# Kernel tuning notes

Hardware: AMD Instinct MI355X
Metric: run time of the kernel (lower is better)

The kernel has to match this reference:

```python
import jax, jax.numpy as jnp
import numpy as np

N, P, C, IMG = 65536, 2048, 3, 256


def setup_inputs() -> dict:
    key = jax.random.key(0)
    k1, k2, k3, k4 = jax.random.split(key, 4)
    X = jax.random.randint(k1, (N, 2), 0, IMG, dtype=jnp.int32)
    pattern_layer = jax.random.randint(k2, (P, 2), 0, IMG, dtype=jnp.int32)
    W2 = jax.random.normal(k3, (C, P), dtype=jnp.float32)
    # sigma >= 1 per module docstring; adapt_sigma yields per-node values
    sigmaSq = jax.random.uniform(k4, (P,), dtype=jnp.float32) * 4.0 + 1.0
    return {"X": X, "pattern_layer": pattern_layer, "W2": W2, "sigmaSq": sigmaSq}


def reference(X, pattern_layer, W2, sigmaSq):
    # Squared L2 distance from each query pixel to each pattern node, [N, P].
    # Coords are small ints, so the expanded form is exact in fp32.
    Xf = X.astype(jnp.float32)
    Pf = pattern_layer.astype(jnp.float32)
    Dsq = ((Xf * Xf).sum(-1)[:, None]
           + (Pf * Pf).sum(-1)[None, :]
           - 2.0 * Xf @ Pf.T)
    # Gaussian RBF with per-node bandwidth sigmaSq, [N, P]
    rbf = jnp.exp(-Dsq / (2.0 * sigmaSq))
    den = rbf.sum(axis=1)                       # [N]
    num = jnp.einsum('np,cp->nc', rbf, W2)      # [N, C]
    return num / den[:, None]
```

## Files before the change

### kernel.cpp

```cpp
#include <hip/hip_runtime.h>
#include <math.h>

#ifndef __has_builtin
#define __has_builtin(x) 0
#endif

#define GRIDC  32
#define NCELL  1024
#define CSHIFT 3
#define RAD    4

#define OFF_A 2048
#define OFF_B 10240
#define WS_NEED_INTS (10240 + 4096)

__device__ __forceinline__ float fast_exp2(float x) {
#if __has_builtin(__builtin_amdgcn_exp2f)
    return __builtin_amdgcn_exp2f(x);
#else
    return exp2f(x);
#endif
}

__device__ __forceinline__ int cell_of(int x, int y) {
    int cx = x >> CSHIFT; cx = cx < 0 ? 0 : (cx > GRIDC - 1 ? GRIDC - 1 : cx);
    int cy = y >> CSHIFT; cy = cy < 0 ? 0 : (cy > GRIDC - 1 ? GRIDC - 1 : cy);
    return (cy << 5) + cx;
}

__global__ __launch_bounds__(1024) void bin_nodes(const int* __restrict__ pat,
        const float* __restrict__ W2, const float* __restrict__ sig,
        int* __restrict__ wsI, int P) {
    __shared__ int cnt[NCELL];
    __shared__ int buf[NCELL];
    const int tid = threadIdx.x;
    cnt[tid] = 0;
    __syncthreads();

    int cell0 = -1, slot0 = 0, cell1 = -1, slot1 = 0;
    if (tid < P) {
        cell0 = cell_of(pat[2 * tid], pat[2 * tid + 1]);
        slot0 = atomicAdd(&cnt[cell0], 1);
    }
    const int p1 = tid + 1024;
    if (p1 < P) {
        cell1 = cell_of(pat[2 * p1], pat[2 * p1 + 1]);
        slot1 = atomicAdd(&cnt[cell1], 1);
    }
    __syncthreads();

    const int c = cnt[tid];
    buf[tid] = c;
    __syncthreads();
    for (int off = 1; off < NCELL; off <<= 1) {
        int t = (tid >= off) ? buf[tid - off] : 0;
        __syncthreads();
        buf[tid] += t;
        __syncthreads();
    }
    const int excl = buf[tid] - c;
    wsI[tid] = excl;
    if (tid == NCELL - 1) wsI[NCELL] = buf[tid];
    cnt[tid] = excl;
    __syncthreads();

    float4* __restrict__ A = (float4*)(wsI + OFF_A);
    float2* __restrict__ B = (float2*)(wsI + OFF_B);
    if (cell0 >= 0) {
        int pos = cnt[cell0] + slot0;
        A[pos] = make_float4((float)pat[2 * tid], (float)pat[2 * tid + 1],
                             -0.7213475204444817f / sig[tid], W2[tid]);
        B[pos] = make_float2(W2[P + tid], W2[2 * P + tid]);
    }
    if (cell1 >= 0) {
        int pos = cnt[cell1] + slot1;
        A[pos] = make_float4((float)pat[2 * p1], (float)pat[2 * p1 + 1],
                             -0.7213475204444817f / sig[p1], W2[p1]);
        B[pos] = make_float2(W2[P + p1], W2[2 * P + p1]);
    }
}

__global__ __launch_bounds__(256) void rbf_win(const int* __restrict__ X,
        const int* __restrict__ wsI, float* __restrict__ out, int N, int P) {
    __shared__ float4 sA[2048];
    __shared__ float2 sB[2048];
    __shared__ int    sst[NCELL + 1];
    __shared__ float4 accb[128];

    const int tid = threadIdx.x;
    const float4* __restrict__ A = (const float4*)(wsI + OFF_A);
    const float2* __restrict__ B = (const float2*)(wsI + OFF_B);
    for (int i = tid; i < P; i += 256) { sA[i] = A[i]; sB[i] = B[i]; }
    for (int i = tid; i < NCELL + 1; i += 256) sst[i] = wsI[i];
    __syncthreads();

    const int half = tid >> 7;
    const int qi   = tid & 127;
    const int n    = blockIdx.x * 128 + qi;
    const bool act = n < N;

    float xf = 0.f, yf = 0.f;
    int cx = 0, cy = 0;
    if (act) {
        int2 xy = ((const int2*)X)[n];
        xf = (float)xy.x; yf = (float)xy.y;
        cx = xy.x >> CSHIFT; cx = cx < 0 ? 0 : (cx > GRIDC - 1 ? GRIDC - 1 : cx);
        cy = xy.y >> CSHIFT; cy = cy < 0 ? 0 : (cy > GRIDC - 1 ? GRIDC - 1 : cy);
    }

    float den = 0.f, a0 = 0.f, a1 = 0.f, a2 = 0.f;
    if (act) {
        const int x0 = cx - RAD < 0 ? 0 : cx - RAD;
        const int x1 = cx + RAD > GRIDC - 1 ? GRIDC - 1 : cx + RAD;
        const int r0 = half ? 5 : 0;
        const int r1 = half ? 9 : 5;
        for (int r = r0; r < r1; ++r) {
            int gy = cy - RAD + r;
            if ((unsigned)gy >= GRIDC) continue;
            int row = gy << 5;
            int k0 = sst[row + x0];
            int k1 = sst[row + x1 + 1];
            for (int k = k0; k < k1; ++k) {
                float4 a = sA[k];
                float2 b = sB[k];
                float dx = xf - a.x;
                float dy = yf - a.y;
                float rr = fast_exp2(fmaf(dy, dy, dx * dx) * a.z);
                den += rr;
                a0 = fmaf(rr, a.w, a0);
                a1 = fmaf(rr, b.x, a1);
                a2 = fmaf(rr, b.y, a2);
            }
        }
    }

    if (half) accb[qi] = make_float4(den, a0, a1, a2);
    __syncthreads();
    if (!half && act) {
        float4 u = accb[qi];
        den += u.x; a0 += u.y; a1 += u.z; a2 += u.w;
        float inv = 1.0f / den;
        out[3 * n + 0] = a0 * inv;
        out[3 * n + 1] = a1 * inv;
        out[3 * n + 2] = a2 * inv;
    }
}

__global__ void pack_nodes(const int* __restrict__ pat, const float* __restrict__ W2,
                           const float* __restrict__ sigmaSq, float* __restrict__ nodes,
                           int P) {
    int p = blockIdx.x * blockDim.x + threadIdx.x;
    if (p >= P) return;
    float* q = nodes + 8 * (size_t)p;
    q[0] = (float)pat[2 * p];
    q[1] = (float)pat[2 * p + 1];
    q[2] = -0.7213475204444817f / sigmaSq[p];
    q[3] = W2[p];
    q[4] = W2[P + p];
    q[5] = W2[2 * P + p];
    q[6] = 0.0f;
    q[7] = 0.0f;
}

__global__ __launch_bounds__(256) void rbf_main_dyn(const int* __restrict__ X,
                                                    const float* __restrict__ nodes,
                                                    float* __restrict__ outp,
                                                    int N, int P) {
    int n = blockIdx.x * 256 + threadIdx.x;
    if (n >= N) return;
    float xn = (float)X[2 * n], yn = (float)X[2 * n + 1];
    float den = 0.f, a0 = 0.f, a1 = 0.f, a2 = 0.f;
    for (int j = 0; j < P; ++j) {
        const float* q = nodes + (size_t)j * 8;
        float dx = xn - q[0], dy = yn - q[1];
        float r = fast_exp2(fmaf(dy, dy, dx * dx) * q[2]);
        den += r;
        a0 = fmaf(r, q[3], a0);
        a1 = fmaf(r, q[4], a1);
        a2 = fmaf(r, q[5], a2);
    }
    outp[3 * n + 0] = a0 / den;
    outp[3 * n + 1] = a1 / den;
    outp[3 * n + 2] = a2 / den;
}

extern "C" void kernel_launch(void* const* d_in, const int* in_sizes, int n_in,
                              void* d_out, int out_size, void* d_ws, size_t ws_size,
                              hipStream_t stream) {
    const int*   X   = (const int*)d_in[0];
    const int*   pat = (const int*)d_in[1];
    const float* W2  = (const float*)d_in[2];
    const float* sig = (const float*)d_in[3];
    float*       out = (float*)d_out;

    const int N = in_sizes[0] / 2;
    const int P = in_sizes[3];

    int* wsI = (int*)d_ws;

    if (P <= 2048 && out_size == 3 * N && ws_size >= WS_NEED_INTS * sizeof(int)) {
        bin_nodes<<<dim3(1), dim3(1024), 0, stream>>>(pat, W2, sig, wsI, P);
        rbf_win<<<dim3((N + 127) / 128), dim3(256), 0, stream>>>(X, wsI, out, N, P);
    } else {
        float* nodes = (float*)d_ws;
        pack_nodes<<<dim3((P + 255) / 256), dim3(256), 0, stream>>>(pat, W2, sig, nodes, P);
        rbf_main_dyn<<<dim3((N + 255) / 256), dim3(256), 0, stream>>>(X, nodes, out, N, P);
    }
}
```

Measured before the change: 80.93 us.

## Fuse node binning into the RBF window kernel, rebuilding bins per block

The single-block binning kernel and its global workspace round-trip are removed. Each block of the windowed RBF kernel now bins all pattern nodes into shared memory on its own: shared-memory atomics for the counts, a 256-wide scan over 4-cell partial sums, then a scatter of the packed node records. This removes one kernel launch and the serial single-block dependency ahead of the main kernel. In exchange, every block repeats the binning work, adds extra barriers, and holds more registers for the per-thread node arrays, which could lower occupancy.

Measured after the change: 76.34 us. 5.7% less time.

```diff
diff --git a/kernel.cpp b/kernel.cpp
--- a/kernel.cpp
+++ b/kernel.cpp
@@ -9,10 +9,6 @@
 #define NCELL  1024
 #define CSHIFT 3
 #define RAD    4
-
-#define OFF_A 2048
-#define OFF_B 10240
-#define WS_NEED_INTS (10240 + 4096)
 
 __device__ __forceinline__ float fast_exp2(float x) {
 #if __has_builtin(__builtin_amdgcn_exp2f)
@@ -28,70 +24,64 @@
     return (cy << 5) + cx;
 }
 
-__global__ __launch_bounds__(1024) void bin_nodes(const int* __restrict__ pat,
-        const float* __restrict__ W2, const float* __restrict__ sig,
-        int* __restrict__ wsI, int P) {
-    __shared__ int cnt[NCELL];
-    __shared__ int buf[NCELL];
+__global__ __launch_bounds__(256) void rbf_fused(const int* __restrict__ X,
+        const int* __restrict__ pat, const float* __restrict__ W2,
+        const float* __restrict__ sig, float* __restrict__ out, int N, int P) {
+    __shared__ float4 sA[2048];
+    __shared__ float2 sB[2048];
+    __shared__ int    sst[NCELL + 1];
+    __shared__ int    part[256];
+    __shared__ float4 accb[128];
+
     const int tid = threadIdx.x;
-    cnt[tid] = 0;
+
+    for (int i = tid; i < NCELL + 1; i += 256) sst[i] = 0;
     __syncthreads();
 
-    int cell0 = -1, slot0 = 0, cell1 = -1, slot1 = 0;
-    if (tid < P) {
-        cell0 = cell_of(pat[2 * tid], pat[2 * tid + 1]);
-        slot0 = atomicAdd(&cnt[cell0], 1);
-    }
-    const int p1 = tid + 1024;
-    if (p1 < P) {
-        cell1 = cell_of(pat[2 * p1], pat[2 * p1 + 1]);
-        slot1 = atomicAdd(&cnt[cell1], 1);
+    int cellr[8], slotr[8], xr[8], yr[8];
+#pragma unroll
+    for (int j = 0; j < 8; ++j) {
+        int p = j * 256 + tid;
+        cellr[j] = -1;
+        if (p < P) {
+            int2 xy = ((const int2*)pat)[p];
+            xr[j] = xy.x; yr[j] = xy.y;
+            int c = cell_of(xy.x, xy.y);
+            cellr[j] = c;
+            slotr[j] = atomicAdd(&sst[c], 1);
+        }
     }
     __syncthreads();
 
-    const int c = cnt[tid];
-    buf[tid] = c;
+    const int c0 = sst[4 * tid], c1 = sst[4 * tid + 1];
+    const int c2 = sst[4 * tid + 2], c3 = sst[4 * tid + 3];
+    const int sum = c0 + c1 + c2 + c3;
+    part[tid] = sum;
     __syncthreads();
-    for (int off = 1; off < NCELL; off <<= 1) {
-        int t = (tid >= off) ? buf[tid - off] : 0;
+    for (int off = 1; off < 256; off <<= 1) {
+        int t = (tid >= off) ? part[tid - off] : 0;
         __syncthreads();
-        buf[tid] += t;
+        part[tid] += t;
         __syncthreads();
     }
-    const int excl = buf[tid] - c;
-    wsI[tid] = excl;
-    if (tid == NCELL - 1) wsI[NCELL] = buf[tid];
-    cnt[tid] = excl;
+    int excl = part[tid] - sum;
+    sst[4 * tid + 0] = excl; excl += c0;
+    sst[4 * tid + 1] = excl; excl += c1;
+    sst[4 * tid + 2] = excl; excl += c2;
+    sst[4 * tid + 3] = excl;
+    if (tid == 255) sst[NCELL] = part[255];
     __syncthreads();
 
-    float4* __restrict__ A = (float4*)(wsI + OFF_A);
-    float2* __restrict__ B = (float2*)(wsI + OFF_B);
-    if (cell0 >= 0) {
-        int pos = cnt[cell0] + slot0;
-        A[pos] = make_float4((float)pat[2 * tid], (float)pat[2 * tid + 1],
-                             -0.7213475204444817f / sig[tid], W2[tid]);
-        B[pos] = make_float2(W2[P + tid], W2[2 * P + tid]);
+#pragma unroll
+    for (int j = 0; j < 8; ++j) {
+        if (cellr[j] >= 0) {
+            int p = j * 256 + tid;
+            int pos = sst[cellr[j]] + slotr[j];
+            sA[pos] = make_float4((float)xr[j], (float)yr[j],
+                                  -0.7213475204444817f / sig[p], W2[p]);
+            sB[pos] = make_float2(W2[P + p], W2[2 * P + p]);
+        }
     }
-    if (cell1 >= 0) {
-        int pos = cnt[cell1] + slot1;
-        A[pos] = make_float4((float)pat[2 * p1], (float)pat[2 * p1 + 1],
-                             -0.7213475204444817f / sig[p1], W2[p1]);
-        B[pos] = make_float2(W2[P + p1], W2[2 * P + p1]);
-    }
-}
-
-__global__ __launch_bounds__(256) void rbf_win(const int* __restrict__ X,
-        const int* __restrict__ wsI, float* __restrict__ out, int N, int P) {
-    __shared__ float4 sA[2048];
-    __shared__ float2 sB[2048];
-    __shared__ int    sst[NCELL + 1];
-    __shared__ float4 accb[128];
-
-    const int tid = threadIdx.x;
-    const float4* __restrict__ A = (const float4*)(wsI + OFF_A);
-    const float2* __restrict__ B = (const float2*)(wsI + OFF_B);
-    for (int i = tid; i < P; i += 256) { sA[i] = A[i]; sB[i] = B[i]; }
-    for (int i = tid; i < NCELL + 1; i += 256) sst[i] = wsI[i];
     __syncthreads();
 
     const int half = tid >> 7;
@@ -196,11 +186,9 @@
     const int N = in_sizes[0] / 2;
     const int P = in_sizes[3];
 
-    int* wsI = (int*)d_ws;
-
-    if (P <= 2048 && out_size == 3 * N && ws_size >= WS_NEED_INTS * sizeof(int)) {
-        bin_nodes<<<dim3(1), dim3(1024), 0, stream>>>(pat, W2, sig, wsI, P);
-        rbf_win<<<dim3((N + 127) / 128), dim3(256), 0, stream>>>(X, wsI, out, N, P);
+    if (P <= 2048 && out_size == 3 * N) {
+        rbf_fused<<<dim3((N + 127) / 128), dim3(256), 0, stream>>>(
+            X, pat, W2, sig, out, N, P);
     } else {
         float* nodes = (float*)d_ws;
         pack_nodes<<<dim3((P + 255) / 256), dim3(256), 0, stream>>>(pat, W2, sig, nodes, P);
```
